# Kernel tuning notes

Measured on AMD Instinct MI355X. Metric: run time of the kernel, lower is better.

Reference implementation:

```python
import jax, jax.numpy as jnp
import numpy as np

N = 20000   # nodes
E = 320000  # edges (before self-loops)
HID = 64    # hidden_dim
H = 4       # attention heads
C = HID     # per-head channels (concat=False -> mean over heads)
CDIM = 8    # contrastive_dim
NEG_SLOPE = 0.2


def setup_inputs() -> dict:
    key = jax.random.key(0)
    ks = jax.random.split(key, 32)
    g = lambda k, shape: (jax.random.normal(k, shape, jnp.float32) * 0.05)
    inp = {
        "x": jax.random.normal(ks[0], (N, 8), jnp.float32),
        "edge_index": jax.random.randint(ks[1], (2, E), 0, N, jnp.int64),
        # lc_encode MLP: 8 -> 32 -> HID
        "W_enc1": g(ks[2], (8, 32)),  "b_enc1": jnp.zeros((32,), jnp.float32),
        "W_enc2": g(ks[3], (32, HID)), "b_enc2": jnp.zeros((HID,), jnp.float32),
        # three GATConv layers: lin (HID -> H*C, no bias), att_src/att_dst (H, C), bias (C,)
        "W_g1": g(ks[4], (HID, H * C)), "as1": g(ks[5], (H, C)), "ad1": g(ks[6], (H, C)), "bg1": jnp.zeros((C,), jnp.float32),
        "W_g2": g(ks[7], (HID, H * C)), "as2": g(ks[8], (H, C)), "ad2": g(ks[9], (H, C)), "bg2": jnp.zeros((C,), jnp.float32),
        "W_g3": g(ks[10], (HID, H * C)), "as3": g(ks[11], (H, C)), "ad3": g(ks[12], (H, C)), "bg3": jnp.zeros((C,), jnp.float32),
        # output MLP: HID -> 64 -> 32 -> CDIM (dropout inactive at eval)
        "W_o1": g(ks[13], (HID, 64)), "b_o1": jnp.zeros((64,), jnp.float32),
        "W_o2": g(ks[14], (64, 32)),  "b_o2": jnp.zeros((32,), jnp.float32),
        "W_o3": g(ks[15], (32, CDIM)), "b_o3": jnp.zeros((CDIM,), jnp.float32),
    }
    return inp


def gat_conv(x, src, dst, n, W, att_src, att_dst, bias):
    # PyG GATConv, heads=H, concat=False (mean over heads), eval mode (no dropout)
    h = (x @ W).reshape(n, H, C)                       # [N,H,C]
    a_src = jnp.einsum('nhc,hc->nh', h, att_src)        # [N,H]
    a_dst = jnp.einsum('nhc,hc->nh', h, att_dst)        # [N,H]
    logits = jax.nn.leaky_relu(a_src[src] + a_dst[dst], NEG_SLOPE)  # [Etot,H]
    m = jax.ops.segment_max(logits, dst, num_segments=n)            # segment softmax (stable)
    e = jnp.exp(logits - m[dst])
    denom = jax.ops.segment_sum(e, dst, num_segments=n)
    alpha = e / (denom[dst] + 1e-16)                    # [Etot,H]
    msg = h[src] * alpha[:, :, None]                    # [Etot,H,C]
    out = jax.ops.segment_sum(msg, dst, num_segments=n) # [N,H,C]
    return out.mean(axis=1) + bias                      # concat=False -> head mean


def reference(x, edge_index, W_enc1, b_enc1, W_enc2, b_enc2,
              W_g1, as1, ad1, bg1, W_g2, as2, ad2, bg2, W_g3, as3, ad3, bg3,
              W_o1, b_o1, W_o2, b_o2, W_o3, b_o3):
    n = x.shape[0]
    loops = jnp.arange(n, dtype=edge_index.dtype)       # GATConv add_self_loops=True
    src = jnp.concatenate([edge_index[0], loops])
    dst = jnp.concatenate([edge_index[1], loops])

    h = jax.nn.elu(jax.nn.elu(x @ W_enc1 + b_enc1) @ W_enc2 + b_enc2)
    h1 = gat_conv(h, src, dst, n, W_g1, as1, ad1, bg1) + h
    h2 = gat_conv(h1, src, dst, n, W_g2, as2, ad2, bg2) + h1
    h3 = gat_conv(h2, src, dst, n, W_g3, as3, ad3, bg3) + h2

    o = jax.nn.elu(h3 @ W_o1 + b_o1)
    o = jax.nn.elu(o @ W_o2 + b_o2)
    return o @ W_o3 + b_o3
```

## Files before the change

kernel.cpp:

```cpp
#include <hip/hip_runtime.h>
#include <cstdint>
#include <cstddef>

#define NEG_SLOPE 0.2f

__device__ __forceinline__ float elu_f(float x) {
    return x > 0.f ? x : expm1f(x);
}

__global__ __launch_bounds__(256) void prep_kernel(
    const int* __restrict__ ei,
    const float* __restrict__ W0, const float* __restrict__ as0, const float* __restrict__ ad0,
    const float* __restrict__ W1, const float* __restrict__ as1, const float* __restrict__ ad1,
    const float* __restrict__ W2, const float* __restrict__ as2, const float* __restrict__ ad2,
    int* __restrict__ cnt, int* __restrict__ ready, int* __restrict__ flag,
    float* __restrict__ vfold, int n) {
    const int b = blockIdx.x, t = threadIdx.x;
    if (b < 79) {
        const int i = b * 256 + t;
        if (i < n) cnt[i] = 0;
        if (b == 0) {
            if (t < 128) ready[t] = 0;
            if (t == 0) {
                int acc = 0;
#pragma unroll
                for (int k = 0; k < 8; ++k) acc |= ei[2 * k + 1];
                flag[0] = (acc == 0) ? 1 : 0;
            }
        }
        return;
    }
    const int e = (b - 79) * 256 + t;
    if (e >= 1536) return;
    const int l = e >> 9, rem = e & 511;
    const int k = rem >> 3, j = rem & 7, h = j & 3;
    const float* W   = (l == 0) ? W0  : (l == 1) ? W1  : W2;
    const float* as_ = (l == 0) ? as0 : (l == 1) ? as1 : as2;
    const float* ad_ = (l == 0) ? ad0 : (l == 1) ? ad1 : ad2;
    const float* av = (j < 4) ? as_ : ad_;
    const float* wr = W + k * 256 + h * 64;
    const float* ar = av + h * 64;
    float s = 0.f;
#pragma unroll 8
    for (int cc = 0; cc < 64; ++cc) s += wr[cc] * ar[cc];
    vfold[l * 512 + k * 8 + j] = s;
}

__global__ void count_kernel(const int* __restrict__ ei, const int* __restrict__ flag,
                             int E, int Etot, int* __restrict__ cnt) {
    int e = blockIdx.x * blockDim.x + threadIdx.x;
    if (e >= Etot) return;
    int d;
    if (e < E) d = flag[0] ? ei[2 * (size_t)(E + e)] : ei[E + e];
    else       d = e - E;
    atomicAdd(&cnt[d], 1);
}

#define SCAN_B 256
__global__ __launch_bounds__(256) void scan_onepass_kernel(
    const int* __restrict__ cnt, int* __restrict__ ready,
    int* __restrict__ rowptr, int* __restrict__ cursor, int n) {
    __shared__ int sd[SCAN_B];
    __shared__ int sred[128];
    __shared__ int s_pref;
    const int b = blockIdx.x, t = threadIdx.x;
    const int g = b * SCAN_B + t;
    const int v = (g < n) ? cnt[g] : 0;
    sd[t] = v;
    __syncthreads();
    for (int off = 1; off < SCAN_B; off <<= 1) {
        int add = (t >= off) ? sd[t - off] : 0;
        __syncthreads();
        sd[t] += add;
        __syncthreads();
    }
    if (t == SCAN_B - 1) atomicExch(&ready[b], sd[SCAN_B - 1] + 1);
    if (t < 128) {
        int pv = 0;
        if (t < b) {
            do { pv = atomicAdd(&ready[t], 0); __builtin_amdgcn_s_sleep(1); } while (pv == 0);
            pv -= 1;
        }
        sred[t] = pv;
    }
    __syncthreads();
    if (t == 0) {
        int s = 0;
#pragma unroll 8
        for (int i = 0; i < 128; ++i) s += sred[i];
        s_pref = s;
    }
    __syncthreads();
    const int pre = s_pref;
    if (g < n) {
        const int e = pre + sd[t];
        rowptr[g + 1] = e;
        cursor[g] = e - v;
        if (g == 0) rowptr[0] = 0;
    }
}

__global__ void fill_kernel(const int* __restrict__ ei, const int* __restrict__ flag,
                            int E, int Etot, int* __restrict__ cursor,
                            int* __restrict__ col) {
    int e = blockIdx.x * blockDim.x + threadIdx.x;
    if (e >= Etot) return;
    int s, d;
    if (e < E) {
        if (flag[0]) { s = ei[2 * (size_t)e]; d = ei[2 * (size_t)(E + e)]; }
        else         { s = ei[e];             d = ei[E + e]; }
    } else {
        s = d = e - E;
    }
    int pos = atomicAdd(&cursor[d], 1);
    col[pos] = s;
}

#define H1STR 68
__global__ __launch_bounds__(256) void encoder_kernel(
    const float* __restrict__ x,
    const float* __restrict__ W1, const float* __restrict__ b1,
    const float* __restrict__ W2, const float* __restrict__ b2,
    const float* __restrict__ vfold0,
    float* __restrict__ h0, float* __restrict__ asrc, float* __restrict__ adst,
    int n_nodes) {
    __shared__ float W1s[256];
    __shared__ float b1s[32];
    __shared__ float W2s[2048];
    __shared__ float b2s[64];
    __shared__ float vsd[512];
    __shared__ float xS[512];
    __shared__ float h1T[32 * H1STR];
    const int t = threadIdx.x;
    const int n0 = blockIdx.x * 64;
    const int rem = n_nodes - n0;

    *(float4*)(W2s + t * 4) = *(const float4*)(W2 + t * 4);
    *(float4*)(W2s + 1024 + t * 4) = *(const float4*)(W2 + 1024 + t * 4);
    if (t < 64)  *(float4*)(W1s + t * 4) = *(const float4*)(W1 + t * 4);
    if (t < 8)   *(float4*)(b1s + t * 4) = *(const float4*)(b1 + t * 4);
    if (t < 16)  *(float4*)(b2s + t * 4) = *(const float4*)(b2 + t * 4);
    if (t < 128) *(float4*)(vsd + t * 4) = *(const float4*)(vfold0 + t * 4);
    if (t < 128) {
        const int fidx = t * 4;
        float4 v = make_float4(0.f, 0.f, 0.f, 0.f);
        if (fidx < rem * 8) v = *(const float4*)(x + (size_t)n0 * 8 + fidx);
        *(float4*)(xS + fidx) = v;
    }
    __syncthreads();

    {
        const int nl = t >> 2;
        const int j0 = (t & 3) * 8;
        const float4 xa = *(const float4*)(xS + nl * 8);
        const float4 xb = *(const float4*)(xS + nl * 8 + 4);
        const float xk[8] = {xa.x, xa.y, xa.z, xa.w, xb.x, xb.y, xb.z, xb.w};
        float a[8];
#pragma unroll
        for (int u = 0; u < 8; ++u) a[u] = b1s[j0 + u];
#pragma unroll
        for (int k = 0; k < 8; ++k) {
            const float4 w0 = *(const float4*)(W1s + k * 32 + j0);
            const float4 w1 = *(const float4*)(W1s + k * 32 + j0 + 4);
            a[0] += xk[k] * w0.x; a[1] += xk[k] * w0.y;
            a[2] += xk[k] * w0.z; a[3] += xk[k] * w0.w;
            a[4] += xk[k] * w1.x; a[5] += xk[k] * w1.y;
            a[6] += xk[k] * w1.z; a[7] += xk[k] * w1.w;
        }
#pragma unroll
        for (int u = 0; u < 8; ++u) h1T[(j0 + u) * H1STR + nl] = elu_f(a[u]);
    }
    __syncthreads();

    const int cg = t & 15;
    const int nq = t >> 4;
    const int c0 = cg * 4;
    float acc[4][4];
#pragma unroll
    for (int i = 0; i < 4; ++i)
#pragma unroll
        for (int c = 0; c < 4; ++c) acc[i][c] = b2s[c0 + c];
#pragma unroll 8
    for (int k = 0; k < 32; ++k) {
        const float4 hv = *(const float4*)(h1T + k * H1STR + nq * 4);
        const float4 wv = *(const float4*)(W2s + k * 64 + c0);
        const float hvv[4] = {hv.x, hv.y, hv.z, hv.w};
#pragma unroll
        for (int i = 0; i < 4; ++i) {
            acc[i][0] += hvv[i] * wv.x; acc[i][1] += hvv[i] * wv.y;
            acc[i][2] += hvv[i] * wv.z; acc[i][3] += hvv[i] * wv.w;
        }
    }
    float o[4][4];
#pragma unroll
    for (int i = 0; i < 4; ++i)
#pragma unroll
        for (int c = 0; c < 4; ++c) o[i][c] = elu_f(acc[i][c]);

#pragma unroll
    for (int i = 0; i < 4; ++i) {
        const int n = n0 + nq * 4 + i;
        if (n < n_nodes)
            *(float4*)(h0 + (size_t)n * 64 + c0) =
                make_float4(o[i][0], o[i][1], o[i][2], o[i][3]);
    }
    float ad[4][8];
#pragma unroll
    for (int i = 0; i < 4; ++i)
#pragma unroll
        for (int jj = 0; jj < 8; ++jj) ad[i][jj] = 0.f;
#pragma unroll
    for (int c = 0; c < 4; ++c) {
        const float4 v0 = *(const float4*)(vsd + (c0 + c) * 8);
        const float4 v1 = *(const float4*)(vsd + (c0 + c) * 8 + 4);
#pragma unroll
        for (int i = 0; i < 4; ++i) {
            ad[i][0] += o[i][c] * v0.x; ad[i][1] += o[i][c] * v0.y;
            ad[i][2] += o[i][c] * v0.z; ad[i][3] += o[i][c] * v0.w;
            ad[i][4] += o[i][c] * v1.x; ad[i][5] += o[i][c] * v1.y;
            ad[i][6] += o[i][c] * v1.z; ad[i][7] += o[i][c] * v1.w;
        }
    }
#pragma unroll
    for (int off = 1; off < 16; off <<= 1) {
#pragma unroll
        for (int i = 0; i < 4; ++i)
#pragma unroll
            for (int jj = 0; jj < 8; ++jj)
                ad[i][jj] += __shfl_xor(ad[i][jj], off);
    }
    if (cg == 0) {
#pragma unroll
        for (int i = 0; i < 4; ++i) {
            const int n = n0 + nq * 4 + i;
            if (n < n_nodes) {
#pragma unroll
                for (int h = 0; h < 4; ++h) {
                    asrc[n * 4 + h] = ad[i][h];
                    adst[n * 4 + h] = ad[i][4 + h];
                }
            }
        }
    }
}

__global__ __launch_bounds__(256) void gat_agg_kernel(
    const float* __restrict__ bin, const float* __restrict__ asrc,
    const float* __restrict__ adst, const int* __restrict__ rowptr,
    const int* __restrict__ col, float* __restrict__ g, int n_nodes) {
    const int grp = threadIdx.x >> 4;
    const int q = threadIdx.x & 15;
    const int n = blockIdx.x * 16 + grp;
    if (n >= n_nodes) return;
    const float4 ad4 = *(const float4*)(adst + (size_t)n * 4);
    const int start = rowptr[n], end = rowptr[n + 1];

    float acc[4][4];
#pragma unroll
    for (int h = 0; h < 4; ++h)
#pragma unroll
        for (int z = 0; z < 4; ++z) acc[h][z] = 0.f;
    float4 den4 = make_float4(0.f, 0.f, 0.f, 0.f);

    for (int base = start; base < end; base += 16) {
        const int cnt = min(16, end - base);
        int c = 0;
        float4 w4 = make_float4(0.f, 0.f, 0.f, 0.f);
        if (base + q < end) {
            c = col[base + q];
            const float4 av = *(const float4*)(asrc + (size_t)c * 4);
            float l0 = av.x + ad4.x; l0 = l0 > 0.f ? l0 : NEG_SLOPE * l0;
            float l1 = av.y + ad4.y; l1 = l1 > 0.f ? l1 : NEG_SLOPE * l1;
            float l2 = av.z + ad4.z; l2 = l2 > 0.f ? l2 : NEG_SLOPE * l2;
            float l3 = av.w + ad4.w; l3 = l3 > 0.f ? l3 : NEG_SLOPE * l3;
            w4.x = __expf(fminf(l0, 60.f));
            w4.y = __expf(fminf(l1, 60.f));
            w4.z = __expf(fminf(l2, 60.f));
            w4.w = __expf(fminf(l3, 60.f));
            den4.x += w4.x; den4.y += w4.y; den4.z += w4.z; den4.w += w4.w;
        }
        int j = 0;
        for (; j + 4 <= cnt; j += 4) {
#pragma unroll
            for (int u = 0; u < 4; ++u) {
                const int s = __shfl(c, j + u, 16);
                const float4 hv = *(const float4*)(bin + (size_t)s * 64 + q * 4);
                const float wx = __shfl(w4.x, j + u, 16);
                const float wy = __shfl(w4.y, j + u, 16);
                const float wz = __shfl(w4.z, j + u, 16);
                const float ww = __shfl(w4.w, j + u, 16);
                acc[0][0] += wx * hv.x; acc[0][1] += wx * hv.y;
                acc[0][2] += wx * hv.z; acc[0][3] += wx * hv.w;
                acc[1][0] += wy * hv.x; acc[1][1] += wy * hv.y;
                acc[1][2] += wy * hv.z; acc[1][3] += wy * hv.w;
                acc[2][0] += wz * hv.x; acc[2][1] += wz * hv.y;
                acc[2][2] += wz * hv.z; acc[2][3] += wz * hv.w;
                acc[3][0] += ww * hv.x; acc[3][1] += ww * hv.y;
                acc[3][2] += ww * hv.z; acc[3][3] += ww * hv.w;
            }
        }
        for (; j < cnt; ++j) {
            const int s = __shfl(c, j, 16);
            const float4 hv = *(const float4*)(bin + (size_t)s * 64 + q * 4);
            const float wx = __shfl(w4.x, j, 16);
            const float wy = __shfl(w4.y, j, 16);
            const float wz = __shfl(w4.z, j, 16);
            const float ww = __shfl(w4.w, j, 16);
            acc[0][0] += wx * hv.x; acc[0][1] += wx * hv.y;
            acc[0][2] += wx * hv.z; acc[0][3] += wx * hv.w;
            acc[1][0] += wy * hv.x; acc[1][1] += wy * hv.y;
            acc[1][2] += wy * hv.z; acc[1][3] += wy * hv.w;
            acc[2][0] += wz * hv.x; acc[2][1] += wz * hv.y;
            acc[2][2] += wz * hv.z; acc[2][3] += wz * hv.w;
            acc[3][0] += ww * hv.x; acc[3][1] += ww * hv.y;
            acc[3][2] += ww * hv.z; acc[3][3] += ww * hv.w;
        }
    }
#pragma unroll
    for (int off = 1; off < 16; off <<= 1) {
        den4.x += __shfl_xor(den4.x, off, 16);
        den4.y += __shfl_xor(den4.y, off, 16);
        den4.z += __shfl_xor(den4.z, off, 16);
        den4.w += __shfl_xor(den4.w, off, 16);
    }
    const float i0 = 1.f / (den4.x + 1e-16f);
    const float i1 = 1.f / (den4.y + 1e-16f);
    const float i2 = 1.f / (den4.z + 1e-16f);
    const float i3 = 1.f / (den4.w + 1e-16f);
    float* gr = g + (size_t)n * 256 + q * 4;
    *(float4*)(gr +   0) = make_float4(acc[0][0]*i0, acc[0][1]*i0, acc[0][2]*i0, acc[0][3]*i0);
    *(float4*)(gr +  64) = make_float4(acc[1][0]*i1, acc[1][1]*i1, acc[1][2]*i1, acc[1][3]*i1);
    *(float4*)(gr + 128) = make_float4(acc[2][0]*i2, acc[2][1]*i2, acc[2][2]*i2, acc[2][3]*i2);
    *(float4*)(gr + 192) = make_float4(acc[3][0]*i3, acc[3][1]*i3, acc[3][2]*i3, acc[3][3]*i3);
}

#define GSTR 132
__global__ __launch_bounds__(256) void gat_post_kernel(
    const float* __restrict__ g, const float* __restrict__ W,
    const float* __restrict__ bias, const float* __restrict__ xin,
    const float* __restrict__ vfold_next, int has_next,
    float* __restrict__ out, float* __restrict__ asrc, float* __restrict__ adst,
    const float* __restrict__ Wm1, const float* __restrict__ bm1,
    const float* __restrict__ Wm2, const float* __restrict__ bm2,
    const float* __restrict__ Wm3, const float* __restrict__ bm3,
    float* __restrict__ mlp_out, int n_nodes) {
    __shared__ float gS[64 * GSTR];
    __shared__ float Wp[128 * 64];
    __shared__ float vN[512];
    const int t = threadIdx.x;
    const int n0 = blockIdx.x * 64;
    const int cg = t & 7;
    const int ng = t >> 3;

    if (has_next && t < 128) *(float4*)(vN + t * 4) = *(const float4*)(vfold_next + t * 4);

    float acc[2][8];
#pragma unroll
    for (int i = 0; i < 2; ++i)
#pragma unroll
        for (int qq = 0; qq < 8; ++qq) acc[i][qq] = 0.f;

    for (int slab = 0; slab < 2; ++slab) {
        __syncthreads();
#pragma unroll
        for (int j = 0; j < 8; ++j) {
            const int idx = j * 256 + t;
            const int nl = idx >> 5;
            const int c4 = idx & 31;
            float4 v = make_float4(0.f, 0.f, 0.f, 0.f);
            if (n0 + nl < n_nodes)
                v = *(const float4*)(g + (size_t)(n0 + nl) * 256 + slab * 128 + c4 * 4);
            *(float4*)(gS + nl * GSTR + c4 * 4) = v;
        }
#pragma unroll
        for (int j = 0; j < 8; ++j) {
            const int f4 = j * 256 + t;
            const int kl = f4 >> 4;
            const int kap = slab * 128 + kl;
            const int h = kap >> 6, kk = kap & 63;
            const int c = (f4 & 15) * 4;
            *(float4*)(Wp + kl * 64 + c) = *(const float4*)(W + kk * 256 + h * 64 + c);
        }
        __syncthreads();
#pragma unroll 4
        for (int kl = 0; kl < 128; ++kl) {
            const float a0 = gS[(ng * 2 + 0) * GSTR + kl];
            const float a1 = gS[(ng * 2 + 1) * GSTR + kl];
            const float4 b0 = *(const float4*)(Wp + kl * 64 + cg * 8);
            const float4 b1 = *(const float4*)(Wp + kl * 64 + cg * 8 + 4);
            acc[0][0] += a0 * b0.x; acc[0][1] += a0 * b0.y;
            acc[0][2] += a0 * b0.z; acc[0][3] += a0 * b0.w;
            acc[0][4] += a0 * b1.x; acc[0][5] += a0 * b1.y;
            acc[0][6] += a0 * b1.z; acc[0][7] += a0 * b1.w;
            acc[1][0] += a1 * b0.x; acc[1][1] += a1 * b0.y;
            acc[1][2] += a1 * b0.z; acc[1][3] += a1 * b0.w;
            acc[1][4] += a1 * b1.x; acc[1][5] += a1 * b1.y;
            acc[1][6] += a1 * b1.z; acc[1][7] += a1 * b1.w;
        }
    }

    const int c0 = cg * 8;
    const float4 bb0 = *(const float4*)(bias + c0);
    const float4 bb1 = *(const float4*)(bias + c0 + 4);
    float o[2][8];
#pragma unroll
    for (int i = 0; i < 2; ++i) {
        const int n = n0 + ng * 2 + i;
        if (n < n_nodes) {
            const float4 x0 = *(const float4*)(xin + (size_t)n * 64 + c0);
            const float4 x1 = *(const float4*)(xin + (size_t)n * 64 + c0 + 4);
            o[i][0] = 0.25f * acc[i][0] + bb0.x + x0.x;
            o[i][1] = 0.25f * acc[i][1] + bb0.y + x0.y;
            o[i][2] = 0.25f * acc[i][2] + bb0.z + x0.z;
            o[i][3] = 0.25f * acc[i][3] + bb0.w + x0.w;
            o[i][4] = 0.25f * acc[i][4] + bb1.x + x1.x;
            o[i][5] = 0.25f * acc[i][5] + bb1.y + x1.y;
            o[i][6] = 0.25f * acc[i][6] + bb1.z + x1.z;
            o[i][7] = 0.25f * acc[i][7] + bb1.w + x1.w;
            if (has_next) {
                *(float4*)(out + (size_t)n * 64 + c0) =
                    make_float4(o[i][0], o[i][1], o[i][2], o[i][3]);
                *(float4*)(out + (size_t)n * 64 + c0 + 4) =
                    make_float4(o[i][4], o[i][5], o[i][6], o[i][7]);
            }
        } else {
#pragma unroll
            for (int qq = 0; qq < 8; ++qq) o[i][qq] = 0.f;
        }
    }

    if (has_next) {
        float pj[2][8];
#pragma unroll
        for (int i = 0; i < 2; ++i)
#pragma unroll
            for (int jj = 0; jj < 8; ++jj) pj[i][jj] = 0.f;
#pragma unroll
        for (int cidx = 0; cidx < 8; ++cidx) {
#pragma unroll
            for (int jj = 0; jj < 8; ++jj) {
                const float vv = vN[(c0 + cidx) * 8 + jj];
                pj[0][jj] += o[0][cidx] * vv;
                pj[1][jj] += o[1][cidx] * vv;
            }
        }
#pragma unroll
        for (int off = 1; off < 8; off <<= 1) {
#pragma unroll
            for (int i = 0; i < 2; ++i)
#pragma unroll
                for (int jj = 0; jj < 8; ++jj)
                    pj[i][jj] += __shfl_xor(pj[i][jj], off);
        }
        if (cg == 0) {
#pragma unroll
            for (int i = 0; i < 2; ++i) {
                const int n = n0 + ng * 2 + i;
                if (n < n_nodes) {
#pragma unroll
                    for (int h = 0; h < 4; ++h) {
                        asrc[n * 4 + h] = pj[i][h];
                        adst[n * 4 + h] = pj[i][4 + h];
                    }
                }
            }
        }
        return;
    }

    __syncthreads();
#pragma unroll
    for (int i = 0; i < 2; ++i) {
        const int nl = ng * 2 + i;
        *(float4*)(gS + nl * GSTR + c0)     = make_float4(o[i][0], o[i][1], o[i][2], o[i][3]);
        *(float4*)(gS + nl * GSTR + c0 + 4) = make_float4(o[i][4], o[i][5], o[i][6], o[i][7]);
    }
    {
#pragma unroll
        for (int j = 0; j < 4; ++j)
            *(float4*)(Wp + (j * 256 + t) * 4) = *(const float4*)(Wm1 + (j * 256 + t) * 4);
#pragma unroll
        for (int j = 0; j < 2; ++j)
            *(float4*)(Wp + 4096 + (j * 256 + t) * 4) = *(const float4*)(Wm2 + (j * 256 + t) * 4);
        if (t < 64) vN[t] = bm1[t];
        else if (t < 96) vN[t] = bm2[t - 64];
        else if (t < 104) vN[t] = bm3[t - 96];
        vN[104 + t] = Wm3[t];
    }
    __syncthreads();
    {
        float a1[2][8];
#pragma unroll
        for (int i = 0; i < 2; ++i)
#pragma unroll
            for (int qq = 0; qq < 8; ++qq) a1[i][qq] = vN[c0 + qq];
#pragma unroll 4
        for (int k = 0; k < 64; ++k) {
            const float h0 = gS[(ng * 2 + 0) * GSTR + k];
            const float h1v = gS[(ng * 2 + 1) * GSTR + k];
            const float4 w0 = *(const float4*)(Wp + k * 64 + c0);
            const float4 w1 = *(const float4*)(Wp + k * 64 + c0 + 4);
            a1[0][0] += h0 * w0.x; a1[0][1] += h0 * w0.y;
            a1[0][2] += h0 * w0.z; a1[0][3] += h0 * w0.w;
            a1[0][4] += h0 * w1.x; a1[0][5] += h0 * w1.y;
            a1[0][6] += h0 * w1.z; a1[0][7] += h0 * w1.w;
            a1[1][0] += h1v * w0.x; a1[1][1] += h1v * w0.y;
            a1[1][2] += h1v * w0.z; a1[1][3] += h1v * w0.w;
            a1[1][4] += h1v * w1.x; a1[1][5] += h1v * w1.y;
            a1[1][6] += h1v * w1.z; a1[1][7] += h1v * w1.w;
        }
#pragma unroll
        for (int i = 0; i < 2; ++i) {
            const int nl = ng * 2 + i;
            float4 v0 = make_float4(elu_f(a1[i][0]), elu_f(a1[i][1]), elu_f(a1[i][2]), elu_f(a1[i][3]));
            float4 v1 = make_float4(elu_f(a1[i][4]), elu_f(a1[i][5]), elu_f(a1[i][6]), elu_f(a1[i][7]));
            *(float4*)(gS + nl * GSTR + 64 + c0)     = v0;
            *(float4*)(gS + nl * GSTR + 64 + c0 + 4) = v1;
        }
    }
    __syncthreads();
    {
        const int cg4 = t & 3;
        const int nn = t >> 2;
        const int cc0 = cg4 * 8;
        float a2[8];
#pragma unroll
        for (int qq = 0; qq < 8; ++qq) a2[qq] = vN[64 + cc0 + qq];
#pragma unroll 4
        for (int j = 0; j < 64; ++j) {
            const float ov = gS[nn * GSTR + 64 + j];
            const float4 w0 = *(const float4*)(Wp + 4096 + j * 32 + cc0);
            const float4 w1 = *(const float4*)(Wp + 4096 + j * 32 + cc0 + 4);
            a2[0] += ov * w0.x; a2[1] += ov * w0.y;
            a2[2] += ov * w0.z; a2[3] += ov * w0.w;
            a2[4] += ov * w1.x; a2[5] += ov * w1.y;
            a2[6] += ov * w1.z; a2[7] += ov * w1.w;
        }
        __syncthreads();
        *(float4*)(gS + nn * GSTR + cc0)     = make_float4(elu_f(a2[0]), elu_f(a2[1]), elu_f(a2[2]), elu_f(a2[3]));
        *(float4*)(gS + nn * GSTR + cc0 + 4) = make_float4(elu_f(a2[4]), elu_f(a2[5]), elu_f(a2[6]), elu_f(a2[7]));
    }
    __syncthreads();
    {
        const int c3 = t & 7;
        const int nq = t >> 3;
#pragma unroll
        for (int i = 0; i < 2; ++i) {
            const int nl = nq * 2 + i;
            const int n = n0 + nl;
            if (n >= n_nodes) continue;
            float a3 = vN[96 + c3];
#pragma unroll 4
            for (int j = 0; j < 32; ++j)
                a3 += gS[nl * GSTR + j] * vN[104 + j * 8 + c3];
            mlp_out[(size_t)n * 8 + c3] = a3;
        }
    }
}

extern "C" void kernel_launch(void* const* d_in, const int* in_sizes, int n_in,
                              void* d_out, int out_size, void* d_ws, size_t ws_size,
                              hipStream_t stream) {
    const float* x     = (const float*)d_in[0];
    const int*   ei    = (const int*)d_in[1];
    const float* Wenc1 = (const float*)d_in[2];
    const float* benc1 = (const float*)d_in[3];
    const float* Wenc2 = (const float*)d_in[4];
    const float* benc2 = (const float*)d_in[5];
    const float* Wg[3]  = {(const float*)d_in[6],  (const float*)d_in[10], (const float*)d_in[14]};
    const float* as_[3] = {(const float*)d_in[7],  (const float*)d_in[11], (const float*)d_in[15]};
    const float* ad_[3] = {(const float*)d_in[8],  (const float*)d_in[12], (const float*)d_in[16]};
    const float* bg[3]  = {(const float*)d_in[9],  (const float*)d_in[13], (const float*)d_in[17]};
    const float* Wo1 = (const float*)d_in[18];
    const float* bo1 = (const float*)d_in[19];
    const float* Wo2 = (const float*)d_in[20];
    const float* bo2 = (const float*)d_in[21];
    const float* Wo3 = (const float*)d_in[22];
    const float* bo3 = (const float*)d_in[23];

    const int N = in_sizes[0] / 8;
    const int E = in_sizes[1] / 2;
    const int Etot = E + N;
    const int nblk = (N + SCAN_B - 1) / SCAN_B;

    float* buf0  = (float*)d_ws;
    float* buf1  = buf0 + (size_t)N * 64;
    float* g     = buf1 + (size_t)N * 64;
    float* asrc  = g + (size_t)N * 256;
    float* adst  = asrc + (size_t)N * 4;
    float* vfold = adst + (size_t)N * 4;
    int* rowptr = (int*)(vfold + 3 * 512);
    int* cursor = rowptr + (N + 2);
    int* cnt    = cursor + N;
    int* ready  = cnt + N;
    int* flag   = ready + 128;
    int* col    = flag + 2;

    prep_kernel<<<nblk + 6, 256, 0, stream>>>(ei,
        Wg[0], as_[0], ad_[0], Wg[1], as_[1], ad_[1], Wg[2], as_[2], ad_[2],
        cnt, ready, flag, vfold, N);
    count_kernel<<<(Etot + 255) / 256, 256, 0, stream>>>(ei, flag, E, Etot, cnt);
    scan_onepass_kernel<<<nblk, SCAN_B, 0, stream>>>(cnt, ready, rowptr, cursor, N);
    fill_kernel<<<(Etot + 255) / 256, 256, 0, stream>>>(ei, flag, E, Etot, cursor, col);

    encoder_kernel<<<(N + 63) / 64, 256, 0, stream>>>(x, Wenc1, benc1, Wenc2, benc2,
                                                      vfold, buf0, asrc, adst, N);

    float* bin = buf0;
    float* bout = buf1;
    for (int l = 0; l < 3; ++l) {
        gat_agg_kernel<<<(N + 15) / 16, 256, 0, stream>>>(bin, asrc, adst, rowptr, col,
                                                          g, N);
        const int has_next = (l < 2) ? 1 : 0;
        gat_post_kernel<<<(N + 63) / 64, 256, 0, stream>>>(
            g, Wg[l], bg[l], bin, vfold + (l + 1 < 3 ? (l + 1) * 512 : 0), has_next,
            bout, asrc, adst,
            Wo1, bo1, Wo2, bo2, Wo3, bo3, (float*)d_out, N);
        float* tmp = bin; bin = bout; bout = tmp;
    }
}
```

Baseline: 286.4 us.

## Fuse GAT aggregation with projection kernel and merge CSR fill into encoder

Merges the per-layer edge aggregation and the dense post-projection into one 512-thread kernel. Aggregated head features stay in shared memory and registers instead of a 256-wide intermediate buffer written to and read back from global memory. Attention score buffers are double-buffered so one layer's blocks can write the next layer's scores while other blocks still read the current ones. The CSR fill kernel and the encoder are also combined into a single launch with partitioned blocks, which cuts launch count but raises register pressure and may lower occupancy in the fused kernel.

After: 282.0 us. Within noise of the previous version (-1.6%).

```diff
diff --git a/kernel.cpp b/kernel.cpp
--- a/kernel.cpp
+++ b/kernel.cpp
@@ -100,30 +100,30 @@
     }
 }
 
-__global__ void fill_kernel(const int* __restrict__ ei, const int* __restrict__ flag,
-                            int E, int Etot, int* __restrict__ cursor,
-                            int* __restrict__ col) {
-    int e = blockIdx.x * blockDim.x + threadIdx.x;
-    if (e >= Etot) return;
-    int s, d;
-    if (e < E) {
-        if (flag[0]) { s = ei[2 * (size_t)e]; d = ei[2 * (size_t)(E + e)]; }
-        else         { s = ei[e];             d = ei[E + e]; }
-    } else {
-        s = d = e - E;
-    }
-    int pos = atomicAdd(&cursor[d], 1);
-    col[pos] = s;
-}
-
 #define H1STR 68
-__global__ __launch_bounds__(256) void encoder_kernel(
+__global__ __launch_bounds__(256) void fillenc_kernel(
+    const int* __restrict__ ei, const int* __restrict__ flag,
+    int E, int Etot, int* __restrict__ cursor, int* __restrict__ col, int FB,
     const float* __restrict__ x,
     const float* __restrict__ W1, const float* __restrict__ b1,
     const float* __restrict__ W2, const float* __restrict__ b2,
     const float* __restrict__ vfold0,
     float* __restrict__ h0, float* __restrict__ asrc, float* __restrict__ adst,
     int n_nodes) {
+    if (blockIdx.x < FB) {
+        const int e = blockIdx.x * 256 + threadIdx.x;
+        if (e >= Etot) return;
+        int s, d;
+        if (e < E) {
+            if (flag[0]) { s = ei[2 * (size_t)e]; d = ei[2 * (size_t)(E + e)]; }
+            else         { s = ei[e];             d = ei[E + e]; }
+        } else {
+            s = d = e - E;
+        }
+        int pos = atomicAdd(&cursor[d], 1);
+        col[pos] = s;
+        return;
+    }
     __shared__ float W1s[256];
     __shared__ float b1s[32];
     __shared__ float W2s[2048];
@@ -132,7 +132,7 @@
     __shared__ float xS[512];
     __shared__ float h1T[32 * H1STR];
     const int t = threadIdx.x;
-    const int n0 = blockIdx.x * 64;
+    const int n0 = (blockIdx.x - FB) * 64;
     const int rem = n_nodes - n0;
 
     *(float4*)(W2s + t * 4) = *(const float4*)(W2 + t * 4);
@@ -244,188 +244,193 @@
     }
 }
 
-__global__ __launch_bounds__(256) void gat_agg_kernel(
+#define GSTR 132
+__global__ __launch_bounds__(512, 2) void gat_fused_kernel(
     const float* __restrict__ bin, const float* __restrict__ asrc,
     const float* __restrict__ adst, const int* __restrict__ rowptr,
-    const int* __restrict__ col, float* __restrict__ g, int n_nodes) {
-    const int grp = threadIdx.x >> 4;
-    const int q = threadIdx.x & 15;
-    const int n = blockIdx.x * 16 + grp;
-    if (n >= n_nodes) return;
-    const float4 ad4 = *(const float4*)(adst + (size_t)n * 4);
-    const int start = rowptr[n], end = rowptr[n + 1];
-
-    float acc[4][4];
-#pragma unroll
-    for (int h = 0; h < 4; ++h)
-#pragma unroll
-        for (int z = 0; z < 4; ++z) acc[h][z] = 0.f;
-    float4 den4 = make_float4(0.f, 0.f, 0.f, 0.f);
-
-    for (int base = start; base < end; base += 16) {
-        const int cnt = min(16, end - base);
-        int c = 0;
-        float4 w4 = make_float4(0.f, 0.f, 0.f, 0.f);
-        if (base + q < end) {
-            c = col[base + q];
-            const float4 av = *(const float4*)(asrc + (size_t)c * 4);
-            float l0 = av.x + ad4.x; l0 = l0 > 0.f ? l0 : NEG_SLOPE * l0;
-            float l1 = av.y + ad4.y; l1 = l1 > 0.f ? l1 : NEG_SLOPE * l1;
-            float l2 = av.z + ad4.z; l2 = l2 > 0.f ? l2 : NEG_SLOPE * l2;
-            float l3 = av.w + ad4.w; l3 = l3 > 0.f ? l3 : NEG_SLOPE * l3;
-            w4.x = __expf(fminf(l0, 60.f));
-            w4.y = __expf(fminf(l1, 60.f));
-            w4.z = __expf(fminf(l2, 60.f));
-            w4.w = __expf(fminf(l3, 60.f));
-            den4.x += w4.x; den4.y += w4.y; den4.z += w4.z; den4.w += w4.w;
-        }
-        int j = 0;
-        for (; j + 4 <= cnt; j += 4) {
-#pragma unroll
-            for (int u = 0; u < 4; ++u) {
-                const int s = __shfl(c, j + u, 16);
-                const float4 hv = *(const float4*)(bin + (size_t)s * 64 + q * 4);
-                const float wx = __shfl(w4.x, j + u, 16);
-                const float wy = __shfl(w4.y, j + u, 16);
-                const float wz = __shfl(w4.z, j + u, 16);
-                const float ww = __shfl(w4.w, j + u, 16);
-                acc[0][0] += wx * hv.x; acc[0][1] += wx * hv.y;
-                acc[0][2] += wx * hv.z; acc[0][3] += wx * hv.w;
-                acc[1][0] += wy * hv.x; acc[1][1] += wy * hv.y;
-                acc[1][2] += wy * hv.z; acc[1][3] += wy * hv.w;
-                acc[2][0] += wz * hv.x; acc[2][1] += wz * hv.y;
-                acc[2][2] += wz * hv.z; acc[2][3] += wz * hv.w;
-                acc[3][0] += ww * hv.x; acc[3][1] += ww * hv.y;
-                acc[3][2] += ww * hv.z; acc[3][3] += ww * hv.w;
-            }
-        }
-        for (; j < cnt; ++j) {
-            const int s = __shfl(c, j, 16);
-            const float4 hv = *(const float4*)(bin + (size_t)s * 64 + q * 4);
-            const float wx = __shfl(w4.x, j, 16);
-            const float wy = __shfl(w4.y, j, 16);
-            const float wz = __shfl(w4.z, j, 16);
-            const float ww = __shfl(w4.w, j, 16);
-            acc[0][0] += wx * hv.x; acc[0][1] += wx * hv.y;
-            acc[0][2] += wx * hv.z; acc[0][3] += wx * hv.w;
-            acc[1][0] += wy * hv.x; acc[1][1] += wy * hv.y;
-            acc[1][2] += wy * hv.z; acc[1][3] += wy * hv.w;
-            acc[2][0] += wz * hv.x; acc[2][1] += wz * hv.y;
-            acc[2][2] += wz * hv.z; acc[2][3] += wz * hv.w;
-            acc[3][0] += ww * hv.x; acc[3][1] += ww * hv.y;
-            acc[3][2] += ww * hv.z; acc[3][3] += ww * hv.w;
-        }
-    }
-#pragma unroll
-    for (int off = 1; off < 16; off <<= 1) {
-        den4.x += __shfl_xor(den4.x, off, 16);
-        den4.y += __shfl_xor(den4.y, off, 16);
-        den4.z += __shfl_xor(den4.z, off, 16);
-        den4.w += __shfl_xor(den4.w, off, 16);
-    }
-    const float i0 = 1.f / (den4.x + 1e-16f);
-    const float i1 = 1.f / (den4.y + 1e-16f);
-    const float i2 = 1.f / (den4.z + 1e-16f);
-    const float i3 = 1.f / (den4.w + 1e-16f);
-    float* gr = g + (size_t)n * 256 + q * 4;
-    *(float4*)(gr +   0) = make_float4(acc[0][0]*i0, acc[0][1]*i0, acc[0][2]*i0, acc[0][3]*i0);
-    *(float4*)(gr +  64) = make_float4(acc[1][0]*i1, acc[1][1]*i1, acc[1][2]*i1, acc[1][3]*i1);
-    *(float4*)(gr + 128) = make_float4(acc[2][0]*i2, acc[2][1]*i2, acc[2][2]*i2, acc[2][3]*i2);
-    *(float4*)(gr + 192) = make_float4(acc[3][0]*i3, acc[3][1]*i3, acc[3][2]*i3, acc[3][3]*i3);
-}
-
-#define GSTR 132
-__global__ __launch_bounds__(256) void gat_post_kernel(
-    const float* __restrict__ g, const float* __restrict__ W,
-    const float* __restrict__ bias, const float* __restrict__ xin,
+    const int* __restrict__ col,
+    const float* __restrict__ W, const float* __restrict__ bias,
     const float* __restrict__ vfold_next, int has_next,
-    float* __restrict__ out, float* __restrict__ asrc, float* __restrict__ adst,
+    float* __restrict__ out,
+    float* __restrict__ nasrc, float* __restrict__ nadst,
     const float* __restrict__ Wm1, const float* __restrict__ bm1,
     const float* __restrict__ Wm2, const float* __restrict__ bm2,
     const float* __restrict__ Wm3, const float* __restrict__ bm3,
     float* __restrict__ mlp_out, int n_nodes) {
     __shared__ float gS[64 * GSTR];
-    __shared__ float Wp[128 * 64];
+    __shared__ float Wp[4096];
     __shared__ float vN[512];
     const int t = threadIdx.x;
     const int n0 = blockIdx.x * 64;
-    const int cg = t & 7;
-    const int ng = t >> 3;
+    const int grp = t >> 4;
+    const int q = t & 15;
+    const int c0 = q * 4;
 
     if (has_next && t < 128) *(float4*)(vN + t * 4) = *(const float4*)(vfold_next + t * 4);
 
-    float acc[2][8];
+    float keep[2][8];
+#pragma unroll
+    for (int i = 0; i < 2; ++i) {
+        const int nl = grp * 2 + i;
+        const int n = n0 + nl;
+        float acc[4][4];
+#pragma unroll
+        for (int h = 0; h < 4; ++h)
+#pragma unroll
+            for (int z = 0; z < 4; ++z) acc[h][z] = 0.f;
+        if (n < n_nodes) {
+            float4 den4 = make_float4(0.f, 0.f, 0.f, 0.f);
+            const float4 ad4 = *(const float4*)(adst + (size_t)n * 4);
+            const int start = rowptr[n], end = rowptr[n + 1];
+            for (int base = start; base < end; base += 16) {
+                const int cnt = min(16, end - base);
+                int c = 0;
+                float4 w4 = make_float4(0.f, 0.f, 0.f, 0.f);
+                if (base + q < end) {
+                    c = col[base + q];
+                    const float4 av = *(const float4*)(asrc + (size_t)c * 4);
+                    float l0 = av.x + ad4.x; l0 = l0 > 0.f ? l0 : NEG_SLOPE * l0;
+                    float l1 = av.y + ad4.y; l1 = l1 > 0.f ? l1 : NEG_SLOPE * l1;
+                    float l2 = av.z + ad4.z; l2 = l2 > 0.f ? l2 : NEG_SLOPE * l2;
+                    float l3 = av.w + ad4.w; l3 = l3 > 0.f ? l3 : NEG_SLOPE * l3;
+                    w4.x = __expf(fminf(l0, 60.f));
+                    w4.y = __expf(fminf(l1, 60.f));
+                    w4.z = __expf(fminf(l2, 60.f));
+                    w4.w = __expf(fminf(l3, 60.f));
+                    den4.x += w4.x; den4.y += w4.y; den4.z += w4.z; den4.w += w4.w;
+                }
+                int j = 0;
+                for (; j + 4 <= cnt; j += 4) {
+#pragma unroll
+                    for (int u = 0; u < 4; ++u) {
+                        const int s = __shfl(c, j + u, 16);
+                        const float4 hv = *(const float4*)(bin + (size_t)s * 64 + q * 4);
+                        const float wx = __shfl(w4.x, j + u, 16);
+                        const float wy = __shfl(w4.y, j + u, 16);
+                        const float wz = __shfl(w4.z, j + u, 16);
+                        const float ww = __shfl(w4.w, j + u, 16);
+                        acc[0][0] += wx * hv.x; acc[0][1] += wx * hv.y;
+                        acc[0][2] += wx * hv.z; acc[0][3] += wx * hv.w;
+                        acc[1][0] += wy * hv.x; acc[1][1] += wy * hv.y;
+                        acc[1][2] += wy * hv.z; acc[1][3] += wy * hv.w;
+                        acc[2][0] += wz * hv.x; acc[2][1] += wz * hv.y;
+                        acc[2][2] += wz * hv.z; acc[2][3] += wz * hv.w;
+                        acc[3][0] += ww * hv.x; acc[3][1] += ww * hv.y;
+                        acc[3][2] += ww * hv.z; acc[3][3] += ww * hv.w;
+                    }
+                }
+                for (; j < cnt; ++j) {
+                    const int s = __shfl(c, j, 16);
+                    const float4 hv = *(const float4*)(bin + (size_t)s * 64 + q * 4);
+                    const float wx = __shfl(w4.x, j, 16);
+                    const float wy = __shfl(w4.y, j, 16);
+                    const float wz = __shfl(w4.z, j, 16);
+                    const float ww = __shfl(w4.w, j, 16);
+                    acc[0][0] += wx * hv.x; acc[0][1] += wx * hv.y;
+                    acc[0][2] += wx * hv.z; acc[0][3] += wx * hv.w;
+                    acc[1][0] += wy * hv.x; acc[1][1] += wy * hv.y;
+                    acc[1][2] += wy * hv.z; acc[1][3] += wy * hv.w;
+                    acc[2][0] += wz * hv.x; acc[2][1] += wz * hv.y;
+                    acc[2][2] += wz * hv.z; acc[2][3] += wz * hv.w;
+                    acc[3][0] += ww * hv.x; acc[3][1] += ww * hv.y;
+                    acc[3][2] += ww * hv.z; acc[3][3] += ww * hv.w;
+                }
+            }
+#pragma unroll
+            for (int off = 1; off < 16; off <<= 1) {
+                den4.x += __shfl_xor(den4.x, off, 16);
+                den4.y += __shfl_xor(den4.y, off, 16);
+                den4.z += __shfl_xor(den4.z, off, 16);
+                den4.w += __shfl_xor(den4.w, off, 16);
+            }
+            const float i0 = 1.f / (den4.x + 1e-16f);
+            const float i1 = 1.f / (den4.y + 1e-16f);
+            const float i2 = 1.f / (den4.z + 1e-16f);
+            const float i3 = 1.f / (den4.w + 1e-16f);
+            *(float4*)(gS + nl * GSTR + c0) =
+                make_float4(acc[0][0] * i0, acc[0][1] * i0, acc[0][2] * i0, acc[0][3] * i0);
+            *(float4*)(gS + nl * GSTR + 64 + c0) =
+                make_float4(acc[1][0] * i1, acc[1][1] * i1, acc[1][2] * i1, acc[1][3] * i1);
+            keep[i][0] = acc[2][0] * i2; keep[i][1] = acc[2][1] * i2;
+            keep[i][2] = acc[2][2] * i2; keep[i][3] = acc[2][3] * i2;
+            keep[i][4] = acc[3][0] * i3; keep[i][5] = acc[3][1] * i3;
+            keep[i][6] = acc[3][2] * i3; keep[i][7] = acc[3][3] * i3;
+        } else {
+            const float4 z4 = make_float4(0.f, 0.f, 0.f, 0.f);
+            *(float4*)(gS + nl * GSTR + c0) = z4;
+            *(float4*)(gS + nl * GSTR + 64 + c0) = z4;
+#pragma unroll
+            for (int u = 0; u < 8; ++u) keep[i][u] = 0.f;
+        }
+    }
+
+    float ga2[2][4];
 #pragma unroll
     for (int i = 0; i < 2; ++i)
 #pragma unroll
-        for (int qq = 0; qq < 8; ++qq) acc[i][qq] = 0.f;
-
-    for (int slab = 0; slab < 2; ++slab) {
-        __syncthreads();
-#pragma unroll
-        for (int j = 0; j < 8; ++j) {
-            const int idx = j * 256 + t;
-            const int nl = idx >> 5;
-            const int c4 = idx & 31;
-            float4 v = make_float4(0.f, 0.f, 0.f, 0.f);
-            if (n0 + nl < n_nodes)
-                v = *(const float4*)(g + (size_t)(n0 + nl) * 256 + slab * 128 + c4 * 4);
-            *(float4*)(gS + nl * GSTR + c4 * 4) = v;
-        }
-#pragma unroll
-        for (int j = 0; j < 8; ++j) {
-            const int f4 = j * 256 + t;
-            const int kl = f4 >> 4;
-            const int kap = slab * 128 + kl;
-            const int h = kap >> 6, kk = kap & 63;
-            const int c = (f4 & 15) * 4;
-            *(float4*)(Wp + kl * 64 + c) = *(const float4*)(W + kk * 256 + h * 64 + c);
-        }
-        __syncthreads();
+        for (int c = 0; c < 4; ++c) ga2[i][c] = 0.f;
+
+#pragma unroll
+    for (int half = 0; half < 2; ++half) {
+        if (half == 1) {
+#pragma unroll
+            for (int i = 0; i < 2; ++i) {
+                const int nl = grp * 2 + i;
+                *(float4*)(gS + nl * GSTR + c0) =
+                    make_float4(keep[i][0], keep[i][1], keep[i][2], keep[i][3]);
+                *(float4*)(gS + nl * GSTR + 64 + c0) =
+                    make_float4(keep[i][4], keep[i][5], keep[i][6], keep[i][7]);
+            }
+        }
+#pragma unroll
+        for (int s = 0; s < 2; ++s) {
+#pragma unroll
+            for (int j = 0; j < 2; ++j) {
+                const int f4 = j * 512 + t;
+                const int kl = f4 >> 4;
+                const int c = (f4 & 15) * 4;
+                const int m = half * 128 + s * 64 + kl;
+                const int h = m >> 6, kk = m & 63;
+                *(float4*)(Wp + kl * 64 + c) = *(const float4*)(W + kk * 256 + h * 64 + c);
+            }
+            __syncthreads();
 #pragma unroll 4
-        for (int kl = 0; kl < 128; ++kl) {
-            const float a0 = gS[(ng * 2 + 0) * GSTR + kl];
-            const float a1 = gS[(ng * 2 + 1) * GSTR + kl];
-            const float4 b0 = *(const float4*)(Wp + kl * 64 + cg * 8);
-            const float4 b1 = *(const float4*)(Wp + kl * 64 + cg * 8 + 4);
-            acc[0][0] += a0 * b0.x; acc[0][1] += a0 * b0.y;
-            acc[0][2] += a0 * b0.z; acc[0][3] += a0 * b0.w;
-            acc[0][4] += a0 * b1.x; acc[0][5] += a0 * b1.y;
-            acc[0][6] += a0 * b1.z; acc[0][7] += a0 * b1.w;
-            acc[1][0] += a1 * b0.x; acc[1][1] += a1 * b0.y;
-            acc[1][2] += a1 * b0.z; acc[1][3] += a1 * b0.w;
-            acc[1][4] += a1 * b1.x; acc[1][5] += a1 * b1.y;
-            acc[1][6] += a1 * b1.z; acc[1][7] += a1 * b1.w;
-        }
-    }
-
-    const int c0 = cg * 8;
-    const float4 bb0 = *(const float4*)(bias + c0);
-    const float4 bb1 = *(const float4*)(bias + c0 + 4);
-    float o[2][8];
+            for (int ks = 0; ks < 64; ks += 4) {
+                const float4 a0 = *(const float4*)(gS + (grp * 2 + 0) * GSTR + s * 64 + ks);
+                const float4 a1 = *(const float4*)(gS + (grp * 2 + 1) * GSTR + s * 64 + ks);
+                const float4 w0 = *(const float4*)(Wp + (ks + 0) * 64 + c0);
+                const float4 w1 = *(const float4*)(Wp + (ks + 1) * 64 + c0);
+                const float4 w2 = *(const float4*)(Wp + (ks + 2) * 64 + c0);
+                const float4 w3 = *(const float4*)(Wp + (ks + 3) * 64 + c0);
+                ga2[0][0] += a0.x * w0.x + a0.y * w1.x + a0.z * w2.x + a0.w * w3.x;
+                ga2[0][1] += a0.x * w0.y + a0.y * w1.y + a0.z * w2.y + a0.w * w3.y;
+                ga2[0][2] += a0.x * w0.z + a0.y * w1.z + a0.z * w2.z + a0.w * w3.z;
+                ga2[0][3] += a0.x * w0.w + a0.y * w1.w + a0.z * w2.w + a0.w * w3.w;
+                ga2[1][0] += a1.x * w0.x + a1.y * w1.x + a1.z * w2.x + a1.w * w3.x;
+                ga2[1][1] += a1.x * w0.y + a1.y * w1.y + a1.z * w2.y + a1.w * w3.y;
+                ga2[1][2] += a1.x * w0.z + a1.y * w1.z + a1.z * w2.z + a1.w * w3.z;
+                ga2[1][3] += a1.x * w0.w + a1.y * w1.w + a1.z * w2.w + a1.w * w3.w;
+            }
+            __syncthreads();
+        }
+    }
+
+    const float4 bb = *(const float4*)(bias + c0);
+    float o[2][4];
 #pragma unroll
     for (int i = 0; i < 2; ++i) {
-        const int n = n0 + ng * 2 + i;
+        const int n = n0 + grp * 2 + i;
         if (n < n_nodes) {
-            const float4 x0 = *(const float4*)(xin + (size_t)n * 64 + c0);
-            const float4 x1 = *(const float4*)(xin + (size_t)n * 64 + c0 + 4);
-            o[i][0] = 0.25f * acc[i][0] + bb0.x + x0.x;
-            o[i][1] = 0.25f * acc[i][1] + bb0.y + x0.y;
-            o[i][2] = 0.25f * acc[i][2] + bb0.z + x0.z;
-            o[i][3] = 0.25f * acc[i][3] + bb0.w + x0.w;
-            o[i][4] = 0.25f * acc[i][4] + bb1.x + x1.x;
-            o[i][5] = 0.25f * acc[i][5] + bb1.y + x1.y;
-            o[i][6] = 0.25f * acc[i][6] + bb1.z + x1.z;
-            o[i][7] = 0.25f * acc[i][7] + bb1.w + x1.w;
-            if (has_next) {
+            const float4 x4 = *(const float4*)(bin + (size_t)n * 64 + c0);
+            o[i][0] = 0.25f * ga2[i][0] + bb.x + x4.x;
+            o[i][1] = 0.25f * ga2[i][1] + bb.y + x4.y;
+            o[i][2] = 0.25f * ga2[i][2] + bb.z + x4.z;
+            o[i][3] = 0.25f * ga2[i][3] + bb.w + x4.w;
+            if (has_next)
                 *(float4*)(out + (size_t)n * 64 + c0) =
                     make_float4(o[i][0], o[i][1], o[i][2], o[i][3]);
-                *(float4*)(out + (size_t)n * 64 + c0 + 4) =
-                    make_float4(o[i][4], o[i][5], o[i][6], o[i][7]);
-            }
         } else {
-#pragma unroll
-            for (int qq = 0; qq < 8; ++qq) o[i][qq] = 0.f;
+            o[i][0] = o[i][1] = o[i][2] = o[i][3] = 0.f;
         }
     }
 
@@ -436,31 +441,34 @@
 #pragma unroll
             for (int jj = 0; jj < 8; ++jj) pj[i][jj] = 0.f;
 #pragma unroll
-        for (int cidx = 0; cidx < 8; ++cidx) {
-#pragma unroll
-            for (int jj = 0; jj < 8; ++jj) {
-                const float vv = vN[(c0 + cidx) * 8 + jj];
-                pj[0][jj] += o[0][cidx] * vv;
-                pj[1][jj] += o[1][cidx] * vv;
-            }
-        }
-#pragma unroll
-        for (int off = 1; off < 8; off <<= 1) {
+        for (int c = 0; c < 4; ++c) {
+            const float4 v0 = *(const float4*)(vN + (c0 + c) * 8);
+            const float4 v1 = *(const float4*)(vN + (c0 + c) * 8 + 4);
+#pragma unroll
+            for (int i = 0; i < 2; ++i) {
+                pj[i][0] += o[i][c] * v0.x; pj[i][1] += o[i][c] * v0.y;
+                pj[i][2] += o[i][c] * v0.z; pj[i][3] += o[i][c] * v0.w;
+                pj[i][4] += o[i][c] * v1.x; pj[i][5] += o[i][c] * v1.y;
+                pj[i][6] += o[i][c] * v1.z; pj[i][7] += o[i][c] * v1.w;
+            }
+        }
+#pragma unroll
+        for (int off = 1; off < 16; off <<= 1) {
 #pragma unroll
             for (int i = 0; i < 2; ++i)
 #pragma unroll
                 for (int jj = 0; jj < 8; ++jj)
                     pj[i][jj] += __shfl_xor(pj[i][jj], off);
         }
-        if (cg == 0) {
+        if (q == 0) {
 #pragma unroll
             for (int i = 0; i < 2; ++i) {
-                const int n = n0 + ng * 2 + i;
+                const int n = n0 + grp * 2 + i;
                 if (n < n_nodes) {
 #pragma unroll
                     for (int h = 0; h < 4; ++h) {
-                        asrc[n * 4 + h] = pj[i][h];
-                        adst[n * 4 + h] = pj[i][4 + h];
+                        nasrc[n * 4 + h] = pj[i][h];
+                        nadst[n * 4 + h] = pj[i][4 + h];
                     }
                 }
             }
@@ -468,87 +476,65 @@
         return;
     }
 
-    __syncthreads();
-#pragma unroll
-    for (int i = 0; i < 2; ++i) {
-        const int nl = ng * 2 + i;
-        *(float4*)(gS + nl * GSTR + c0)     = make_float4(o[i][0], o[i][1], o[i][2], o[i][3]);
-        *(float4*)(gS + nl * GSTR + c0 + 4) = make_float4(o[i][4], o[i][5], o[i][6], o[i][7]);
-    }
+#pragma unroll
+    for (int i = 0; i < 2; ++i)
+        *(float4*)(gS + (grp * 2 + i) * GSTR + c0) =
+            make_float4(o[i][0], o[i][1], o[i][2], o[i][3]);
+#pragma unroll
+    for (int j = 0; j < 2; ++j)
+        *(float4*)(Wp + (j * 512 + t) * 4) = *(const float4*)(Wm1 + (j * 512 + t) * 4);
+    if (t < 64) vN[t] = bm1[t];
+    else if (t < 96) vN[t] = bm2[t - 64];
+    else if (t < 104) vN[t] = bm3[t - 96];
+    if (t < 256) vN[104 + t] = Wm3[t];
+    __syncthreads();
     {
-#pragma unroll
-        for (int j = 0; j < 4; ++j)
-            *(float4*)(Wp + (j * 256 + t) * 4) = *(const float4*)(Wm1 + (j * 256 + t) * 4);
-#pragma unroll
-        for (int j = 0; j < 2; ++j)
-            *(float4*)(Wp + 4096 + (j * 256 + t) * 4) = *(const float4*)(Wm2 + (j * 256 + t) * 4);
-        if (t < 64) vN[t] = bm1[t];
-        else if (t < 96) vN[t] = bm2[t - 64];
-        else if (t < 104) vN[t] = bm3[t - 96];
-        vN[104 + t] = Wm3[t];
-    }
-    __syncthreads();
-    {
-        float a1[2][8];
-#pragma unroll
-        for (int i = 0; i < 2; ++i)
-#pragma unroll
-            for (int qq = 0; qq < 8; ++qq) a1[i][qq] = vN[c0 + qq];
+        const int ng = t >> 3;
+        const int cm0 = (t & 7) * 8;
+        float a1[8];
+#pragma unroll
+        for (int u = 0; u < 8; ++u) a1[u] = vN[cm0 + u];
 #pragma unroll 4
         for (int k = 0; k < 64; ++k) {
-            const float h0 = gS[(ng * 2 + 0) * GSTR + k];
-            const float h1v = gS[(ng * 2 + 1) * GSTR + k];
-            const float4 w0 = *(const float4*)(Wp + k * 64 + c0);
-            const float4 w1 = *(const float4*)(Wp + k * 64 + c0 + 4);
-            a1[0][0] += h0 * w0.x; a1[0][1] += h0 * w0.y;
-            a1[0][2] += h0 * w0.z; a1[0][3] += h0 * w0.w;
-            a1[0][4] += h0 * w1.x; a1[0][5] += h0 * w1.y;
-            a1[0][6] += h0 * w1.z; a1[0][7] += h0 * w1.w;
-            a1[1][0] += h1v * w0.x; a1[1][1] += h1v * w0.y;
-            a1[1][2] += h1v * w0.z; a1[1][3] += h1v * w0.w;
-            a1[1][4] += h1v * w1.x; a1[1][5] += h1v * w1.y;
-            a1[1][6] += h1v * w1.z; a1[1][7] += h1v * w1.w;
-        }
-#pragma unroll
-        for (int i = 0; i < 2; ++i) {
-            const int nl = ng * 2 + i;
-            float4 v0 = make_float4(elu_f(a1[i][0]), elu_f(a1[i][1]), elu_f(a1[i][2]), elu_f(a1[i][3]));
-            float4 v1 = make_float4(elu_f(a1[i][4]), elu_f(a1[i][5]), elu_f(a1[i][6]), elu_f(a1[i][7]));
-            *(float4*)(gS + nl * GSTR + 64 + c0)     = v0;
-            *(float4*)(gS + nl * GSTR + 64 + c0 + 4) = v1;
-        }
-    }
+            const float hv = gS[ng * GSTR + k];
+            const float4 w0 = *(const float4*)(Wp + k * 64 + cm0);
+            const float4 w1 = *(const float4*)(Wp + k * 64 + cm0 + 4);
+            a1[0] += hv * w0.x; a1[1] += hv * w0.y;
+            a1[2] += hv * w0.z; a1[3] += hv * w0.w;
+            a1[4] += hv * w1.x; a1[5] += hv * w1.y;
+            a1[6] += hv * w1.z; a1[7] += hv * w1.w;
+        }
+        *(float4*)(gS + ng * GSTR + 64 + cm0) =
+            make_float4(elu_f(a1[0]), elu_f(a1[1]), elu_f(a1[2]), elu_f(a1[3]));
+        *(float4*)(gS + ng * GSTR + 64 + cm0 + 4) =
+            make_float4(elu_f(a1[4]), elu_f(a1[5]), elu_f(a1[6]), elu_f(a1[7]));
+    }
+    __syncthreads();
+    *(float4*)(Wp + t * 4) = *(const float4*)(Wm2 + t * 4);
     __syncthreads();
     {
-        const int cg4 = t & 3;
-        const int nn = t >> 2;
-        const int cc0 = cg4 * 8;
-        float a2[8];
-#pragma unroll
-        for (int qq = 0; qq < 8; ++qq) a2[qq] = vN[64 + cc0 + qq];
+        const int nn = t >> 3;
+        const int cc0 = (t & 7) * 4;
+        float a2[4];
+#pragma unroll
+        for (int u = 0; u < 4; ++u) a2[u] = vN[64 + cc0 + u];
 #pragma unroll 4
         for (int j = 0; j < 64; ++j) {
             const float ov = gS[nn * GSTR + 64 + j];
-            const float4 w0 = *(const float4*)(Wp + 4096 + j * 32 + cc0);
-            const float4 w1 = *(const float4*)(Wp + 4096 + j * 32 + cc0 + 4);
-            a2[0] += ov * w0.x; a2[1] += ov * w0.y;
-            a2[2] += ov * w0.z; a2[3] += ov * w0.w;
-            a2[4] += ov * w1.x; a2[5] += ov * w1.y;
-            a2[6] += ov * w1.z; a2[7] += ov * w1.w;
+            const float4 w = *(const float4*)(Wp + j * 32 + cc0);
+            a2[0] += ov * w.x; a2[1] += ov * w.y;
+            a2[2] += ov * w.z; a2[3] += ov * w.w;
         }
         __syncthreads();
-        *(float4*)(gS + nn * GSTR + cc0)     = make_float4(elu_f(a2[0]), elu_f(a2[1]), elu_f(a2[2]), elu_f(a2[3]));
-        *(float4*)(gS + nn * GSTR + cc0 + 4) = make_float4(elu_f(a2[4]), elu_f(a2[5]), elu_f(a2[6]), elu_f(a2[7]));
+        *(float4*)(gS + nn * GSTR + cc0) =
+            make_float4(elu_f(a2[0]), elu_f(a2[1]), elu_f(a2[2]), elu_f(a2[3]));
     }
     __syncthreads();
     {
+        const int nl = t >> 3;
         const int c3 = t & 7;
-        const int nq = t >> 3;
-#pragma unroll
-        for (int i = 0; i < 2; ++i) {
-            const int nl = nq * 2 + i;
-            const int n = n0 + nl;
-            if (n >= n_nodes) continue;
+        const int n = n0 + nl;
+        if (n < n_nodes) {
             float a3 = vN[96 + c3];
 #pragma unroll 4
             for (int j = 0; j < 32; ++j)
@@ -582,13 +568,16 @@
     const int E = in_sizes[1] / 2;
     const int Etot = E + N;
     const int nblk = (N + SCAN_B - 1) / SCAN_B;
+    const int FB = (Etot + 255) / 256;
+    const int NB64 = (N + 63) / 64;
 
     float* buf0  = (float*)d_ws;
     float* buf1  = buf0 + (size_t)N * 64;
-    float* g     = buf1 + (size_t)N * 64;
-    float* asrc  = g + (size_t)N * 256;
-    float* adst  = asrc + (size_t)N * 4;
-    float* vfold = adst + (size_t)N * 4;
+    float* asA   = buf1 + (size_t)N * 64;
+    float* adA   = asA + (size_t)N * 4;
+    float* asB   = adA + (size_t)N * 4;
+    float* adB   = asB + (size_t)N * 4;
+    float* vfold = adB + (size_t)N * 4;
     int* rowptr = (int*)(vfold + 3 * 512);
     int* cursor = rowptr + (N + 2);
     int* cnt    = cursor + N;
@@ -601,21 +590,17 @@
         cnt, ready, flag, vfold, N);
     count_kernel<<<(Etot + 255) / 256, 256, 0, stream>>>(ei, flag, E, Etot, cnt);
     scan_onepass_kernel<<<nblk, SCAN_B, 0, stream>>>(cnt, ready, rowptr, cursor, N);
-    fill_kernel<<<(Etot + 255) / 256, 256, 0, stream>>>(ei, flag, E, Etot, cursor, col);
-
-    encoder_kernel<<<(N + 63) / 64, 256, 0, stream>>>(x, Wenc1, benc1, Wenc2, benc2,
-                                                      vfold, buf0, asrc, adst, N);
-
-    float* bin = buf0;
-    float* bout = buf1;
-    for (int l = 0; l < 3; ++l) {
-        gat_agg_kernel<<<(N + 15) / 16, 256, 0, stream>>>(bin, asrc, adst, rowptr, col,
-                                                          g, N);
-        const int has_next = (l < 2) ? 1 : 0;
-        gat_post_kernel<<<(N + 63) / 64, 256, 0, stream>>>(
-            g, Wg[l], bg[l], bin, vfold + (l + 1 < 3 ? (l + 1) * 512 : 0), has_next,
-            bout, asrc, adst,
-            Wo1, bo1, Wo2, bo2, Wo3, bo3, (float*)d_out, N);
-        float* tmp = bin; bin = bout; bout = tmp;
-    }
+    fillenc_kernel<<<FB + NB64, 256, 0, stream>>>(ei, flag, E, Etot, cursor, col, FB,
+                                                  x, Wenc1, benc1, Wenc2, benc2,
+                                                  vfold, buf0, asA, adA, N);
+
+    gat_fused_kernel<<<NB64, 512, 0, stream>>>(
+        buf0, asA, adA, rowptr, col, Wg[0], bg[0], vfold + 512, 1,
+        buf1, asB, adB, Wo1, bo1, Wo2, bo2, Wo3, bo3, (float*)d_out, N);
+    gat_fused_kernel<<<NB64, 512, 0, stream>>>(
+        buf1, asB, adB, rowptr, col, Wg[1], bg[1], vfold + 1024, 1,
+        buf0, asA, adA, Wo1, bo1, Wo2, bo2, Wo3, bo3, (float*)d_out, N);
+    gat_fused_kernel<<<NB64, 512, 0, stream>>>(
+        buf0, asA, adA, rowptr, col, Wg[2], bg[2], vfold, 0,
+        buf1, asB, adB, Wo1, bo1, Wo2, bo2, Wo3, bo3, (float*)d_out, N);
 }
```
